# Kernel tuning notes

Measured on AMD Instinct MI355X. Metric: run time of the kernel, lower is better.

The kernel has to match this reference:

```python
import jax, jax.numpy as jnp
import numpy as np

B, CIN, COUT, KH, KW, H, W = 32, 64, 64, 3, 3, 128, 128
STRIDE = (1, 1)
PADDING = [(1, 1), (1, 1)]


def setup_inputs() -> dict:
    key = jax.random.key(0)
    k1, k2, k3, k4 = jax.random.split(key, 4)
    x = jax.random.normal(k1, (B, CIN, H, W), dtype=jnp.float32)
    cov = jax.random.uniform(k2, (B,), dtype=jnp.float32)
    # kaiming-normal fan_out init: std = sqrt(2 / (cout*kh*kw))
    std = np.sqrt(2.0 / (COUT * KH * KW)).astype(np.float32)
    W_0 = jax.random.normal(k3, (COUT, CIN, KH, KW), dtype=jnp.float32) * std
    W_1 = jax.random.normal(k4, (COUT, CIN, KH, KW), dtype=jnp.float32) * std
    return {"x": x, "cov": cov, "W_0": W_0, "W_1": W_1}


def reference(x, cov, W_0, W_1):
    # per-sample kernel: W_0 + cov[i] * W_1  -> [B, COUT, CIN, KH, KW]
    kernels = W_0[None] + cov[:, None, None, None, None] * W_1[None]

    def conv_one(xi, k):
        # xi: [CIN, H, W], k: [COUT, CIN, KH, KW]
        out = jax.lax.conv_general_dilated(
            xi[None], k, window_strides=STRIDE, padding=PADDING,
            dimension_numbers=("NCHW", "OIHW", "NCHW"))
        return out[0]

    return jax.vmap(conv_one)(x, kernels)  # [B, COUT, H, W]
```

## Files before the change

kernel.cpp:

```cpp
#include <hip/hip_runtime.h>
#include <stdint.h>

#define B_   32
#define CIN  64
#define COUT 64
#define H_   128
#define W_   128
#define HP   130
#define WP   130

typedef __bf16 bf16x8 __attribute__((ext_vector_type(8)));
typedef float  f32x4  __attribute__((ext_vector_type(4)));

__device__ inline unsigned short f2bf(float f) {
  union { float f; unsigned u; } uf; uf.f = f;
  unsigned u = uf.u;
  unsigned r = 0x7FFFu + ((u >> 16) & 1u);
  return (unsigned short)((u + r) >> 16);
}

__global__ __launch_bounds__(256) void prep_w(const float* __restrict__ W0,
                                              const float* __restrict__ W1,
                                              const float* __restrict__ cov,
                                              unsigned short* __restrict__ Wb) {
  int g  = blockIdx.x * 256 + threadIdx.x;
  int ci = g & 63;
  int co = (g >> 6) & 63;
  int v  = g >> 12;
  int b  = v / 9;
  int p  = v - b * 9;
  int widx = (co * CIN + ci) * 9 + p;
  float val = W0[widx] + cov[b] * W1[widx];
  Wb[g] = f2bf(val);
}

__global__ __launch_bounds__(256) void zero_pad(unsigned short* __restrict__ Xt) {
  int b = blockIdx.y;
  int i = blockIdx.x * 256 + threadIdx.x;
  size_t base = (size_t)b * HP * WP * 64;
  if (i < 8320) {
    Xt[base + i] = 0;
  } else if (i < 16640) {
    Xt[base + (size_t)129 * WP * 64 + (i - 8320)] = 0;
  } else {
    int j = i - 16640;
    int hh   = 1 + (j >> 7);
    int side = (j >> 6) & 1;
    int cc   = j & 63;
    Xt[base + ((size_t)hh * WP + side * 129) * 64 + cc] = 0;
  }
}

__global__ __launch_bounds__(256) void prep_x(const float* __restrict__ X,
                                              unsigned short* __restrict__ Xt) {
  __shared__ unsigned short T[64][66];
  int bid = blockIdx.x;
  int wt = bid & 1;
  int h  = (bid >> 1) & 127;
  int b  = bid >> 8;
  int t  = threadIdx.x;
  int wlane = t & 63;
  int g0 = t >> 6;
  int w0 = wt * 64;

  const float* src = X + (((size_t)b * CIN) * H_ + h) * W_ + w0 + wlane;
  for (int ci = g0; ci < 64; ci += 4) {
    T[ci][wlane] = f2bf(src[(size_t)ci * (H_ * W_)]);
  }
  __syncthreads();

  int ci = t & 63;
  for (int wi = g0; wi < 64; wi += 4) {
    int wpp = w0 + wi + 1;
    int blk = (ci >> 3) ^ (wpp & 7);
    size_t base = (((size_t)b * HP + (h + 1)) * WP + wpp) * 64;
    Xt[base + blk * 8 + (ci & 7)] = T[ci][wi];
  }
}

__global__ __launch_bounds__(256, 2) void conv_main(
    const unsigned short* __restrict__ Xt,
    const unsigned short* __restrict__ Wb,
    float* __restrict__ out) {
  __shared__ __align__(16) unsigned short Xs[4 * WP * 64];

  int tile = blockIdx.x;
  int b  = tile >> 6;
  int h0 = (tile & 63) * 2;
  int t  = threadIdx.x;
  int w  = t >> 6;
  int l  = t & 63;

  {
    const int4* s4 = (const int4*)(Xt + ((size_t)b * HP + h0) * WP * 64);
    int4* d4 = (int4*)Xs;
    for (int k = t; k < 4160; k += 256) d4[k] = s4[k];
  }
  __syncthreads();

  int lh = l & 15;
  int q  = l >> 4;

  f32x4 acc[4][4];
  #pragma unroll
  for (int i = 0; i < 4; i++)
    #pragma unroll
    for (int j = 0; j < 4; j++) acc[i][j] = (f32x4){0.f, 0.f, 0.f, 0.f};

  int rbase[4], cbase[4];
  #pragma unroll
  for (int nt = 0; nt < 4; nt++) {
    int p = w * 64 + nt * 16 + lh;
    rbase[nt] = p >> 7;
    cbase[nt] = p & 127;
  }

  const unsigned short* wbase = Wb + (size_t)b * 9 * 64 * 64;

  for (int kh = 0; kh < 3; kh++) {
    for (int kw = 0; kw < 3; kw++) {
      const unsigned short* wk = wbase + (kh * 3 + kw) * 64 * 64;
      bf16x8 af[2][4], bfr[2][4];
      #pragma unroll
      for (int ck = 0; ck < 2; ck++)
        #pragma unroll
        for (int mt = 0; mt < 4; mt++)
          af[ck][mt] = *(const bf16x8*)(wk + (mt * 16 + lh) * 64 + ck * 32 + q * 8);
      #pragma unroll
      for (int ck = 0; ck < 2; ck++)
        #pragma unroll
        for (int nt = 0; nt < 4; nt++) {
          int r = rbase[nt] + kh;
          int c = cbase[nt] + kw;
          int blk = (ck * 4 + q) ^ (c & 7);
          bfr[ck][nt] = *(const bf16x8*)(Xs + (r * WP + c) * 64 + blk * 8);
        }
      #pragma unroll
      for (int ck = 0; ck < 2; ck++)
        #pragma unroll
        for (int mt = 0; mt < 4; mt++)
          #pragma unroll
          for (int nt = 0; nt < 4; nt++)
            acc[mt][nt] = __builtin_amdgcn_mfma_f32_16x16x32_bf16(
                af[ck][mt], bfr[ck][nt], acc[mt][nt], 0, 0, 0);
    }
  }

  #pragma unroll
  for (int mt = 0; mt < 4; mt++) {
    int coutb = mt * 16 + q * 4;
    #pragma unroll
    for (int nt = 0; nt < 4; nt++) {
      int oh = h0 + rbase[nt];
      int ow = cbase[nt];
      #pragma unroll
      for (int r = 0; r < 4; r++) {
        int cout = coutb + r;
        out[(((size_t)b * COUT + cout) * H_ + oh) * W_ + ow] = acc[mt][nt][r];
      }
    }
  }
}

extern "C" void kernel_launch(void* const* d_in, const int* in_sizes, int n_in,
                              void* d_out, int out_size, void* d_ws, size_t ws_size,
                              hipStream_t stream) {
  const float* x   = (const float*)d_in[0];
  const float* cov = (const float*)d_in[1];
  const float* W0  = (const float*)d_in[2];
  const float* W1  = (const float*)d_in[3];
  float* out = (float*)d_out;

  unsigned short* Xt = (unsigned short*)d_ws;
  unsigned short* Wb = (unsigned short*)((char*)d_ws + (size_t)B_ * HP * WP * 64 * 2);

  prep_w  <<<dim3(4608),     dim3(256), 0, stream>>>(W0, W1, cov, Wb);
  zero_pad<<<dim3(129, 32),  dim3(256), 0, stream>>>(Xt);
  prep_x  <<<dim3(8192),     dim3(256), 0, stream>>>(x, Xt);
  conv_main<<<dim3(2048),    dim3(256), 0, stream>>>(Xt, Wb, out);
}
```

Before: 338.9 us.

## Fuse input transpose, bf16 conversion and padding into conv kernel

Drops the separate zero_pad and prep_x kernels. The conv kernel now loads its four fp32 input rows directly, converts them to bf16, and writes them into swizzled shared memory, zeroing the padding rows and columns inline. This removes the global round trip of the transposed, padded input and two kernel launches. In exchange each input row is read by two neighbouring tiles, adding redundant loads and conversion work inside the main kernel.

```diff
diff --git a/kernel.cpp b/kernel.cpp
--- a/kernel.cpp
+++ b/kernel.cpp
@@ -6,17 +6,16 @@
 #define COUT 64
 #define H_   128
 #define W_   128
-#define HP   130
 #define WP   130
 
 typedef __bf16 bf16x8 __attribute__((ext_vector_type(8)));
 typedef float  f32x4  __attribute__((ext_vector_type(4)));
 
-__device__ inline unsigned short f2bf(float f) {
+__device__ inline unsigned int f2bf(float f) {
   union { float f; unsigned u; } uf; uf.f = f;
   unsigned u = uf.u;
   unsigned r = 0x7FFFu + ((u >> 16) & 1u);
-  return (unsigned short)((u + r) >> 16);
+  return (u + r) >> 16;
 }
 
 __global__ __launch_bounds__(256) void prep_w(const float* __restrict__ W0,
@@ -31,55 +30,11 @@
   int p  = v - b * 9;
   int widx = (co * CIN + ci) * 9 + p;
   float val = W0[widx] + cov[b] * W1[widx];
-  Wb[g] = f2bf(val);
+  Wb[g] = (unsigned short)f2bf(val);
 }
 
-__global__ __launch_bounds__(256) void zero_pad(unsigned short* __restrict__ Xt) {
-  int b = blockIdx.y;
-  int i = blockIdx.x * 256 + threadIdx.x;
-  size_t base = (size_t)b * HP * WP * 64;
-  if (i < 8320) {
-    Xt[base + i] = 0;
-  } else if (i < 16640) {
-    Xt[base + (size_t)129 * WP * 64 + (i - 8320)] = 0;
-  } else {
-    int j = i - 16640;
-    int hh   = 1 + (j >> 7);
-    int side = (j >> 6) & 1;
-    int cc   = j & 63;
-    Xt[base + ((size_t)hh * WP + side * 129) * 64 + cc] = 0;
-  }
-}
-
-__global__ __launch_bounds__(256) void prep_x(const float* __restrict__ X,
-                                              unsigned short* __restrict__ Xt) {
-  __shared__ unsigned short T[64][66];
-  int bid = blockIdx.x;
-  int wt = bid & 1;
-  int h  = (bid >> 1) & 127;
-  int b  = bid >> 8;
-  int t  = threadIdx.x;
-  int wlane = t & 63;
-  int g0 = t >> 6;
-  int w0 = wt * 64;
-
-  const float* src = X + (((size_t)b * CIN) * H_ + h) * W_ + w0 + wlane;
-  for (int ci = g0; ci < 64; ci += 4) {
-    T[ci][wlane] = f2bf(src[(size_t)ci * (H_ * W_)]);
-  }
-  __syncthreads();
-
-  int ci = t & 63;
-  for (int wi = g0; wi < 64; wi += 4) {
-    int wpp = w0 + wi + 1;
-    int blk = (ci >> 3) ^ (wpp & 7);
-    size_t base = (((size_t)b * HP + (h + 1)) * WP + wpp) * 64;
-    Xt[base + blk * 8 + (ci & 7)] = T[ci][wi];
-  }
-}
-
-__global__ __launch_bounds__(256, 2) void conv_main(
-    const unsigned short* __restrict__ Xt,
+__global__ __launch_bounds__(256, 2) void conv_fused(
+    const float* __restrict__ X,
     const unsigned short* __restrict__ Wb,
     float* __restrict__ out) {
   __shared__ __align__(16) unsigned short Xs[4 * WP * 64];
@@ -88,13 +43,42 @@
   int b  = tile >> 6;
   int h0 = (tile & 63) * 2;
   int t  = threadIdx.x;
-  int w  = t >> 6;
+  int wv = t >> 6;
   int l  = t & 63;
 
+  unsigned short* dst_row = Xs + wv * WP * 64;
+
   {
-    const int4* s4 = (const int4*)(Xt + ((size_t)b * HP + h0) * WP * 64);
-    int4* d4 = (int4*)Xs;
-    for (int k = t; k < 4160; k += 256) d4[k] = s4[k];
+    unsigned int* d32 = (unsigned int*)dst_row;
+    if (l < 32) d32[l] = 0u;
+    else        d32[129 * 32 + (l - 32)] = 0u;
+  }
+
+  int ih = h0 - 1 + wv;
+  if (ih < 0 || ih > 127) {
+    int4 z = {0, 0, 0, 0};
+    int4* d = (int4*)(dst_row + 64);
+    #pragma unroll
+    for (int k = 0; k < 16; k++) d[k * 64 + l] = z;
+  } else {
+    const float* src = X + (((size_t)b * CIN) * H_ + ih) * W_;
+    int w1 = l + 1, w2 = l + 65;
+    unsigned short* p1 = dst_row + w1 * 64;
+    unsigned short* p2 = dst_row + w2 * 64;
+    #pragma unroll 4
+    for (int ci = 0; ci < 64; ci += 2) {
+      const float* s0 = src + (size_t)ci * (H_ * W_);
+      float a0 = s0[l];
+      float a1 = s0[H_ * W_ + l];
+      float b0 = s0[64 + l];
+      float b1 = s0[H_ * W_ + 64 + l];
+      unsigned int lo = f2bf(a0) | (f2bf(a1) << 16);
+      unsigned int hi = f2bf(b0) | (f2bf(b1) << 16);
+      int blk1 = (ci >> 3) ^ (w1 & 7);
+      int blk2 = (ci >> 3) ^ (w2 & 7);
+      *(unsigned int*)(p1 + blk1 * 8 + (ci & 7)) = lo;
+      *(unsigned int*)(p2 + blk2 * 8 + (ci & 7)) = hi;
+    }
   }
   __syncthreads();
 
@@ -110,7 +94,7 @@
   int rbase[4], cbase[4];
   #pragma unroll
   for (int nt = 0; nt < 4; nt++) {
-    int p = w * 64 + nt * 16 + lh;
+    int p = wv * 64 + nt * 16 + lh;
     rbase[nt] = p >> 7;
     cbase[nt] = p & 127;
   }
@@ -171,11 +155,8 @@
   const float* W1  = (const float*)d_in[3];
   float* out = (float*)d_out;
 
-  unsigned short* Xt = (unsigned short*)d_ws;
-  unsigned short* Wb = (unsigned short*)((char*)d_ws + (size_t)B_ * HP * WP * 64 * 2);
+  unsigned short* Wb = (unsigned short*)d_ws;
 
-  prep_w  <<<dim3(4608),     dim3(256), 0, stream>>>(W0, W1, cov, Wb);
-  zero_pad<<<dim3(129, 32),  dim3(256), 0, stream>>>(Xt);
-  prep_x  <<<dim3(8192),     dim3(256), 0, stream>>>(x, Xt);
-  conv_main<<<dim3(2048),    dim3(256), 0, stream>>>(Xt, Wb, out);
+  prep_w   <<<dim3(4608), dim3(256), 0, stream>>>(W0, W1, cov, Wb);
+  conv_fused<<<dim3(2048), dim3(256), 0, stream>>>(x, Wb, out);
 }
```

Measured after the change: 302.7 us. 10.7% less time.
